# Kernel tuning notes

Measured on AMD Instinct MI355X. Metric: run time of the kernel, lower is better.

The kernel has to match this reference:

```python
import jax, jax.numpy as jnp
import numpy as np

B, T, N_EMBD, HEAD = 4, 4096, 1024, 64


def setup_inputs() -> dict:
    key = jax.random.key(0)
    kx, kk, kq, kv = jax.random.split(key, 4)
    x = jax.random.normal(kx, (B, T, N_EMBD), dtype=jnp.float32)
    s = 1.0 / np.sqrt(N_EMBD)  # init scale so activations stay O(1)
    Wk = jax.random.normal(kk, (N_EMBD, HEAD), dtype=jnp.float32) * s
    Wq = jax.random.normal(kq, (N_EMBD, HEAD), dtype=jnp.float32) * s
    Wv = jax.random.normal(kv, (N_EMBD, HEAD), dtype=jnp.float32) * s
    return {"x": x, "Wk": Wk, "Wq": Wq, "Wv": Wv}


def reference(x, Wk, Wq, Wv):
    Bd, Td, C = x.shape
    k = jnp.einsum('btc,ch->bth', x, Wk)
    q = jnp.einsum('btc,ch->bth', x, Wq)
    v = jnp.einsum('btc,ch->bth', x, Wv)
    # scores scaled by C**-0.5 where C = n_embd (as in the source, not head_size)
    w = jnp.einsum('bth,bsh->bts', q, k) * (C ** -0.5)
    causal = jnp.tril(jnp.ones((Td, Td), dtype=bool))  # [T, T]
    w = jnp.where(causal, w, -jnp.inf)
    w = jax.nn.softmax(w, axis=-1)
    out = jnp.einsum('bts,bsh->bth', w, v)  # [B, T, head_size]
    return out
```

## Files before the change

### kernel.cpp

```cpp
#include <hip/hip_runtime.h>
#include <cmath>

#define NB 4
#define NT 4096
#define NC 1024
#define NH 64
#define SCALE 0.03125f
#define MFIX 3.0f
#define LOG2E 1.4426950408889634f
#define QE 1048576

typedef __attribute__((ext_vector_type(8))) short v8s;
typedef __attribute__((ext_vector_type(4))) float f32x4;

static __device__ __forceinline__ ushort f2bf(float x) {
    union { float f; uint u; } c; c.f = x;
    return (ushort)((c.u + 0x7FFF + ((c.u >> 16) & 1)) >> 16);
}
static __device__ __forceinline__ uint pk2bf(float hi_f, float lo_f) {
    uint uh = __float_as_uint(hi_f) + 0x8000u;
    uint ul = __float_as_uint(lo_f) + 0x8000u;
    return __builtin_amdgcn_perm(uh, ul, 0x07060302u);
}

__global__ __launch_bounds__(256) void prep_kernel(
    const float* __restrict__ Wk, const float* __restrict__ Wq,
    const float* __restrict__ Wv, ushort* __restrict__ Wb)
{
    const int g    = blockIdx.x * 256 + threadIdx.x;
    const int lane = g & 63;
    const int kc   = (g >> 6) & 31;
    const int nt   = g >> 11;
    const int n    = nt * 16 + (lane & 15);
    const float* W = (n < 64) ? Wq : (n < 128) ? Wk : Wv;
    const int col  = n & 63;
    const int k0   = kc * 32 + ((lane >> 4) << 3);
    ushort t8[8];
    #pragma unroll
    for (int j = 0; j < 8; ++j)
        t8[j] = f2bf(W[(k0 + j) * 64 + col]);
    *(uint4*)(Wb + (size_t)g * 8) = *(const uint4*)t8;
}

#define PPAD 72

__global__ __launch_bounds__(256) void proj_kernel(
    const float* __restrict__ x, const ushort* __restrict__ Wb,
    ushort* __restrict__ qpack, ushort* __restrict__ kpack,
    ushort* __restrict__ vpack)
{
    __shared__ __align__(16) ushort As[2][32 * PPAD];
    __shared__ __align__(16) ushort Cs[32][200];

    const int tid  = threadIdx.x;
    const int w    = tid >> 6;
    const int lane = tid & 63;
    const int ln   = lane & 15;
    const int quad = lane >> 4;
    const long r0  = (long)blockIdx.x * 32;

    const int arow = tid >> 3, acol = (tid & 7) * 8;
    const float* xs = x + (r0 + arow) * NC + acol;

    const ushort* wb0 = Wb + (size_t)(w * 3 + 0) * 16384 + lane * 8;
    const ushort* wb1 = Wb + (size_t)(w * 3 + 1) * 16384 + lane * 8;
    const ushort* wb2 = Wb + (size_t)(w * 3 + 2) * 16384 + lane * 8;

    f32x4 acc[2][3];
    #pragma unroll
    for (int s = 0; s < 2; ++s)
        #pragma unroll
        for (int nt = 0; nt < 3; ++nt) acc[s][nt] = (f32x4){0.f,0.f,0.f,0.f};

    float4 f0 = *(const float4*)(xs);
    float4 f1 = *(const float4*)(xs + 4);
    float4 g0 = *(const float4*)(xs + 64);
    float4 g1 = *(const float4*)(xs + 68);
    v8s b[3][2];
    b[0][0] = *(const v8s*)(wb0);       b[0][1] = *(const v8s*)(wb0 + 512);
    b[1][0] = *(const v8s*)(wb1);       b[1][1] = *(const v8s*)(wb1 + 512);
    b[2][0] = *(const v8s*)(wb2);       b[2][1] = *(const v8s*)(wb2 + 512);
    {
        uint4 p = { pk2bf(f0.y, f0.x), pk2bf(f0.w, f0.z),
                    pk2bf(f1.y, f1.x), pk2bf(f1.w, f1.z) };
        *(uint4*)(&As[0][arow * PPAD + acol]) = p;
    }
    __syncthreads();

    int buf = 0;
    #pragma unroll
    for (int it = 0; it < 16; ++it) {
        float4 h0, h1;
        v8s nb[3][2];
        if (it < 14) {
            const int k2 = (it + 2) * 64;
            h0 = *(const float4*)(xs + k2);
            h1 = *(const float4*)(xs + k2 + 4);
        }
        if (it < 15) {
            const int off = (it + 1) * 1024;
            nb[0][0] = *(const v8s*)(wb0 + off); nb[0][1] = *(const v8s*)(wb0 + off + 512);
            nb[1][0] = *(const v8s*)(wb1 + off); nb[1][1] = *(const v8s*)(wb1 + off + 512);
            nb[2][0] = *(const v8s*)(wb2 + off); nb[2][1] = *(const v8s*)(wb2 + off + 512);
        }

        #pragma unroll
        for (int s = 0; s < 2; ++s) {
            const ushort* ap = &As[buf][(s * 16 + ln) * PPAD + quad * 8];
            v8s a0 = *(const v8s*)(ap);
            v8s a1 = *(const v8s*)(ap + 32);
            #pragma unroll
            for (int nt = 0; nt < 3; ++nt) {
                acc[s][nt] = __builtin_amdgcn_mfma_f32_16x16x32_bf16(a0, b[nt][0], acc[s][nt], 0, 0, 0);
                acc[s][nt] = __builtin_amdgcn_mfma_f32_16x16x32_bf16(a1, b[nt][1], acc[s][nt], 0, 0, 0);
            }
        }

        if (it < 15) {
            uint4 p = { pk2bf(g0.y, g0.x), pk2bf(g0.w, g0.z),
                        pk2bf(g1.y, g1.x), pk2bf(g1.w, g1.z) };
            *(uint4*)(&As[buf ^ 1][arow * PPAD + acol]) = p;
            #pragma unroll
            for (int nt = 0; nt < 3; ++nt) {
                b[nt][0] = nb[nt][0];
                b[nt][1] = nb[nt][1];
            }
        }
        if (it < 14) { g0 = h0; g1 = h1; }
        __syncthreads();
        buf ^= 1;
    }

    #pragma unroll
    for (int s = 0; s < 2; ++s)
        #pragma unroll
        for (int nt = 0; nt < 3; ++nt)
            #pragma unroll
            for (int r = 0; r < 4; ++r)
                Cs[s * 16 + quad * 4 + r][(w * 3 + nt) * 16 + ln] = f2bf(acc[s][nt][r]);
    __syncthreads();

    const int b_blk = (int)(r0 >> 12);
    const int t_loc = (int)(r0 & 4095);
    const int kt    = t_loc >> 6;
    const int kcb   = (t_loc >> 5) & 1;
    const int qt16a = t_loc >> 4;

    {
        const int f = tid >> 6, sx = f >> 1, kc = f & 1, lp = tid & 63;
        const int lnp = lp & 15, qdp = lp >> 4;
        const size_t fid = ((size_t)(b_blk * 256 + qt16a + sx) * 2 + kc);
        uint4 uq = *(const uint4*)(&Cs[sx * 16 + lnp][kc * 32 + qdp * 8]);
        *(uint4*)(qpack + fid * 512 + lp * 8) = uq;
        uint4 uk = *(const uint4*)(&Cs[sx * 16 + lnp][64 + kc * 32 + qdp * 8]);
        *(uint4*)(kpack + fid * 512 + lp * 8) = uk;
    }
    {
        const int td = tid >> 6, lp = tid & 63;
        const int lnv = lp & 15, qg = lp >> 4;
        ushort t8[8];
        #pragma unroll
        for (int j = 0; j < 8; ++j)
            t8[j] = Cs[qg * 8 + j][128 + td * 16 + lnv];
        const size_t fv = ((size_t)(b_blk * 64 + kt) * 2 + kcb) * 4 + td;
        *(uint4*)(vpack + fv * 512 + lp * 8) = *(const uint4*)t8;
    }
}

#define LPAD 40

__global__ __launch_bounds__(1024) void attn_kernel(
    const ushort* __restrict__ qpack, const ushort* __restrict__ kpack,
    const ushort* __restrict__ vpack, float* __restrict__ out)
{
    __shared__ __align__(16) ushort Ps[16][32 * LPAD];
    __shared__ __align__(16) float Obuf[8][32][68];
    __shared__ float Lbuf[8][32];

    const int id = blockIdx.x;
    const int j  = id >> 2;
    const int b  = id & 3;

    const int tid  = threadIdx.x;
    const int w    = tid >> 6;
    const int lane = tid & 63;
    const int ln   = lane & 15;
    const int quad = lane >> 4;

    const ushort* qpb = qpack + (size_t)b * 256 * 2 * 512 + lane * 8;
    const ushort* kpb = kpack + (size_t)b * 256 * 2 * 512 + lane * 8;
    const ushort* vpb = vpack + (size_t)b * 128 * 4 * 512 + lane * 8;

    ushort* Pw = &Ps[w][0];

    #pragma unroll
    for (int ph = 0; ph < 2; ++ph) {
        const int jp = ph ? (127 - j) : j;
        const int q0 = jp * 32;

        v8s qf[2][2];
        #pragma unroll
        for (int s = 0; s < 2; ++s) {
            qf[s][0] = *(const v8s*)(qpb + ((size_t)((jp * 2 + s) * 2 + 0)) * 512);
            qf[s][1] = *(const v8s*)(qpb + ((size_t)((jp * 2 + s) * 2 + 1)) * 512);
        }

        f32x4 o[2][4];
        #pragma unroll
        for (int s = 0; s < 2; ++s)
            #pragma unroll
            for (int td = 0; td < 4; ++td) o[s][td] = (f32x4){0.f,0.f,0.f,0.f};
        float l[2] = {0.f, 0.f};

        for (int kk = w; kk <= jp; kk += 16) {
            const ushort* kfb = kpb + (size_t)kk * 4 * 512;
            const ushort* vfb = vpb + (size_t)kk * 4 * 512;
            v8s K[4], V[4];
            #pragma unroll
            for (int i = 0; i < 4; ++i) K[i] = *(const v8s*)(kfb + i * 512);
            #pragma unroll
            for (int i = 0; i < 4; ++i) V[i] = *(const v8s*)(vfb + i * 512);
            const bool diag = (kk == jp);

            #pragma unroll
            for (int tk = 0; tk < 2; ++tk) {
                const int keybase = kk * 32 + tk * 16 + quad * 4;
                #pragma unroll
                for (int s = 0; s < 2; ++s) {
                    f32x4 acc = (f32x4){0.f,0.f,0.f,0.f};
                    acc = __builtin_amdgcn_mfma_f32_16x16x32_bf16(K[tk * 2 + 0], qf[s][0], acc, 0, 0, 0);
                    acc = __builtin_amdgcn_mfma_f32_16x16x32_bf16(K[tk * 2 + 1], qf[s][1], acc, 0, 0, 0);
                    const int qg = q0 + s * 16 + ln;
                    float p[4];
                    #pragma unroll
                    for (int r = 0; r < 4; ++r) {
                        float e = fmaf(acc[r], SCALE * LOG2E, -MFIX * LOG2E);
                        if (diag && (keybase + r > qg)) e = -1e30f;
                        p[r] = __builtin_amdgcn_exp2f(e);
                        l[s] += p[r];
                    }
                    uint2 pw = { pk2bf(p[1], p[0]), pk2bf(p[3], p[2]) };
                    *(uint2*)(&Pw[(s * 16 + ln) * LPAD + tk * 16 + quad * 4]) = pw;
                }
            }

            #pragma unroll
            for (int s = 0; s < 2; ++s) {
                v8s pf = *(const v8s*)(&Pw[(s * 16 + ln) * LPAD + quad * 8]);
                #pragma unroll
                for (int td = 0; td < 4; ++td)
                    o[s][td] = __builtin_amdgcn_mfma_f32_16x16x32_bf16(pf, V[td], o[s][td], 0, 0, 0);
            }
        }

        #pragma unroll
        for (int s = 0; s < 2; ++s) {
            l[s] += __shfl_xor(l[s], 16);
            l[s] += __shfl_xor(l[s], 32);
        }

        if (w >= 8) {
            #pragma unroll
            for (int s = 0; s < 2; ++s) {
                #pragma unroll
                for (int td = 0; td < 4; ++td)
                    #pragma unroll
                    for (int r = 0; r < 4; ++r)
                        Obuf[w - 8][s * 16 + quad * 4 + r][td * 16 + ln] = o[s][td][r];
                if (quad == 0) Lbuf[w - 8][s * 16 + ln] = l[s];
            }
        }
        __syncthreads();

        if (w < 8) {
            #pragma unroll
            for (int s = 0; s < 2; ++s) {
                l[s] += Lbuf[w][s * 16 + ln];
                #pragma unroll
                for (int td = 0; td < 4; ++td)
                    #pragma unroll
                    for (int r = 0; r < 4; ++r) {
                        float m = o[s][td][r] + Obuf[w][s * 16 + quad * 4 + r][td * 16 + ln];
                        Obuf[w][s * 16 + quad * 4 + r][td * 16 + ln] = m;
                    }
                if (quad == 0) Lbuf[w][s * 16 + ln] = l[s];
            }
        }
        __syncthreads();

        {
            const int qr = tid >> 5;
            const int h0 = (tid & 31) * 2;
            float s0 = 0.f, s1 = 0.f, Ls = 0.f;
            #pragma unroll
            for (int ww = 0; ww < 8; ++ww) {
                const float* Or = &Obuf[ww][qr][h0];
                s0 += Or[0]; s1 += Or[1];
                Ls += Lbuf[ww][qr];
            }
            const float inv = 1.0f / Ls;
            float2 r = { s0 * inv, s1 * inv };
            *(float2*)(out + ((size_t)b * NT + q0 + qr) * NH + h0) = r;
        }
        __syncthreads();
    }
}

extern "C" void kernel_launch(void* const* d_in, const int* in_sizes, int n_in,
                              void* d_out, int out_size, void* d_ws, size_t ws_size,
                              hipStream_t stream)
{
    const float* x  = (const float*)d_in[0];
    const float* Wk = (const float*)d_in[1];
    const float* Wq = (const float*)d_in[2];
    const float* Wv = (const float*)d_in[3];
    float* out = (float*)d_out;

    char* wsb = (char*)d_ws;
    ushort* qpack = (ushort*)wsb;
    ushort* kpack = qpack + QE;
    ushort* vpack = kpack + QE;
    ushort* Wb    = vpack + QE;

    prep_kernel<<<96, 256, 0, stream>>>(Wk, Wq, Wv, Wb);
    proj_kernel<<<NB * NT / 32, 256, 0, stream>>>(x, Wb, qpack, kpack, vpack);
    attn_kernel<<<64 * NB, 1024, 0, stream>>>(qpack, kpack, vpack, out);
}
```

Measured before the change: 127.8 us.

## Split attention into one query tile per 512-thread block with longest-first ordering

Instead of 256 blocks of 1024 threads that each handle a pair of query tiles (j and 127-j), the attention kernel now launches 512 blocks of 512 threads, each owning a single 32-row query tile. Blocks are ordered so the heaviest causal tiles are scheduled first, with a mirrored mapping for the second half. The cross-wave reduction now spans 8 waves and uses float4 output stores. The aim is finer-grained scheduling, higher occupancy via launch_bounds(512,4), and fewer barriers. The cost is more blocks and per-block setup, plus load balance that depends on the hardware scheduler instead of explicit pairing.

```diff
diff --git a/kernel.cpp b/kernel.cpp
--- a/kernel.cpp
+++ b/kernel.cpp
@@ -169,17 +169,19 @@
 
 #define LPAD 40
 
-__global__ __launch_bounds__(1024) void attn_kernel(
+__global__ __launch_bounds__(512, 4) void attn_kernel(
     const ushort* __restrict__ qpack, const ushort* __restrict__ kpack,
     const ushort* __restrict__ vpack, float* __restrict__ out)
 {
-    __shared__ __align__(16) ushort Ps[16][32 * LPAD];
-    __shared__ __align__(16) float Obuf[8][32][68];
-    __shared__ float Lbuf[8][32];
+    __shared__ __align__(16) ushort Ps[8][32 * LPAD];
+    __shared__ __align__(16) float Obuf[4][32][68];
+    __shared__ float Lbuf[4][32];
 
     const int id = blockIdx.x;
-    const int j  = id >> 2;
-    const int b  = id & 3;
+    const int r  = (id < 256) ? id : 767 - id;
+    const int jp = 127 - (r >> 2);
+    const int b  = r & 3;
+    const int q0 = jp * 32;
 
     const int tid  = threadIdx.x;
     const int w    = tid >> 6;
@@ -193,116 +195,110 @@
 
     ushort* Pw = &Ps[w][0];
 
-    #pragma unroll
-    for (int ph = 0; ph < 2; ++ph) {
-        const int jp = ph ? (127 - j) : j;
-        const int q0 = jp * 32;
-
-        v8s qf[2][2];
+    v8s qf[2][2];
+    #pragma unroll
+    for (int s = 0; s < 2; ++s) {
+        qf[s][0] = *(const v8s*)(qpb + ((size_t)((jp * 2 + s) * 2 + 0)) * 512);
+        qf[s][1] = *(const v8s*)(qpb + ((size_t)((jp * 2 + s) * 2 + 1)) * 512);
+    }
+
+    f32x4 o[2][4];
+    #pragma unroll
+    for (int s = 0; s < 2; ++s)
+        #pragma unroll
+        for (int td = 0; td < 4; ++td) o[s][td] = (f32x4){0.f,0.f,0.f,0.f};
+    float l[2] = {0.f, 0.f};
+
+    for (int kk = w; kk <= jp; kk += 8) {
+        const ushort* kfb = kpb + (size_t)kk * 4 * 512;
+        const ushort* vfb = vpb + (size_t)kk * 4 * 512;
+        v8s K[4], V[4];
+        #pragma unroll
+        for (int i = 0; i < 4; ++i) K[i] = *(const v8s*)(kfb + i * 512);
+        #pragma unroll
+        for (int i = 0; i < 4; ++i) V[i] = *(const v8s*)(vfb + i * 512);
+        const bool diag = (kk == jp);
+
+        #pragma unroll
+        for (int tk = 0; tk < 2; ++tk) {
+            const int keybase = kk * 32 + tk * 16 + quad * 4;
+            #pragma unroll
+            for (int s = 0; s < 2; ++s) {
+                f32x4 acc = (f32x4){0.f,0.f,0.f,0.f};
+                acc = __builtin_amdgcn_mfma_f32_16x16x32_bf16(K[tk * 2 + 0], qf[s][0], acc, 0, 0, 0);
+                acc = __builtin_amdgcn_mfma_f32_16x16x32_bf16(K[tk * 2 + 1], qf[s][1], acc, 0, 0, 0);
+                const int qg = q0 + s * 16 + ln;
+                float p[4];
+                #pragma unroll
+                for (int rr = 0; rr < 4; ++rr) {
+                    float e = fmaf(acc[rr], SCALE * LOG2E, -MFIX * LOG2E);
+                    if (diag && (keybase + rr > qg)) e = -1e30f;
+                    p[rr] = __builtin_amdgcn_exp2f(e);
+                    l[s] += p[rr];
+                }
+                uint2 pw = { pk2bf(p[1], p[0]), pk2bf(p[3], p[2]) };
+                *(uint2*)(&Pw[(s * 16 + ln) * LPAD + tk * 16 + quad * 4]) = pw;
+            }
+        }
+
         #pragma unroll
         for (int s = 0; s < 2; ++s) {
-            qf[s][0] = *(const v8s*)(qpb + ((size_t)((jp * 2 + s) * 2 + 0)) * 512);
-            qf[s][1] = *(const v8s*)(qpb + ((size_t)((jp * 2 + s) * 2 + 1)) * 512);
-        }
-
-        f32x4 o[2][4];
-        #pragma unroll
-        for (int s = 0; s < 2; ++s)
-            #pragma unroll
-            for (int td = 0; td < 4; ++td) o[s][td] = (f32x4){0.f,0.f,0.f,0.f};
-        float l[2] = {0.f, 0.f};
-
-        for (int kk = w; kk <= jp; kk += 16) {
-            const ushort* kfb = kpb + (size_t)kk * 4 * 512;
-            const ushort* vfb = vpb + (size_t)kk * 4 * 512;
-            v8s K[4], V[4];
-            #pragma unroll
-            for (int i = 0; i < 4; ++i) K[i] = *(const v8s*)(kfb + i * 512);
-            #pragma unroll
-            for (int i = 0; i < 4; ++i) V[i] = *(const v8s*)(vfb + i * 512);
-            const bool diag = (kk == jp);
-
-            #pragma unroll
-            for (int tk = 0; tk < 2; ++tk) {
-                const int keybase = kk * 32 + tk * 16 + quad * 4;
+            v8s pf = *(const v8s*)(&Pw[(s * 16 + ln) * LPAD + quad * 8]);
+            #pragma unroll
+            for (int td = 0; td < 4; ++td)
+                o[s][td] = __builtin_amdgcn_mfma_f32_16x16x32_bf16(pf, V[td], o[s][td], 0, 0, 0);
+        }
+    }
+
+    #pragma unroll
+    for (int s = 0; s < 2; ++s) {
+        l[s] += __shfl_xor(l[s], 16);
+        l[s] += __shfl_xor(l[s], 32);
+    }
+
+    if (w >= 4) {
+        #pragma unroll
+        for (int s = 0; s < 2; ++s) {
+            #pragma unroll
+            for (int td = 0; td < 4; ++td)
                 #pragma unroll
-                for (int s = 0; s < 2; ++s) {
-                    f32x4 acc = (f32x4){0.f,0.f,0.f,0.f};
-                    acc = __builtin_amdgcn_mfma_f32_16x16x32_bf16(K[tk * 2 + 0], qf[s][0], acc, 0, 0, 0);
-                    acc = __builtin_amdgcn_mfma_f32_16x16x32_bf16(K[tk * 2 + 1], qf[s][1], acc, 0, 0, 0);
-                    const int qg = q0 + s * 16 + ln;
-                    float p[4];
-                    #pragma unroll
-                    for (int r = 0; r < 4; ++r) {
-                        float e = fmaf(acc[r], SCALE * LOG2E, -MFIX * LOG2E);
-                        if (diag && (keybase + r > qg)) e = -1e30f;
-                        p[r] = __builtin_amdgcn_exp2f(e);
-                        l[s] += p[r];
-                    }
-                    uint2 pw = { pk2bf(p[1], p[0]), pk2bf(p[3], p[2]) };
-                    *(uint2*)(&Pw[(s * 16 + ln) * LPAD + tk * 16 + quad * 4]) = pw;
+                for (int rr = 0; rr < 4; ++rr)
+                    Obuf[w - 4][s * 16 + quad * 4 + rr][td * 16 + ln] = o[s][td][rr];
+            if (quad == 0) Lbuf[w - 4][s * 16 + ln] = l[s];
+        }
+    }
+    __syncthreads();
+
+    if (w < 4) {
+        #pragma unroll
+        for (int s = 0; s < 2; ++s) {
+            l[s] += Lbuf[w][s * 16 + ln];
+            #pragma unroll
+            for (int td = 0; td < 4; ++td)
+                #pragma unroll
+                for (int rr = 0; rr < 4; ++rr) {
+                    float m = o[s][td][rr] + Obuf[w][s * 16 + quad * 4 + rr][td * 16 + ln];
+                    Obuf[w][s * 16 + quad * 4 + rr][td * 16 + ln] = m;
                 }
-            }
-
-            #pragma unroll
-            for (int s = 0; s < 2; ++s) {
-                v8s pf = *(const v8s*)(&Pw[(s * 16 + ln) * LPAD + quad * 8]);
-                #pragma unroll
-                for (int td = 0; td < 4; ++td)
-                    o[s][td] = __builtin_amdgcn_mfma_f32_16x16x32_bf16(pf, V[td], o[s][td], 0, 0, 0);
-            }
-        }
-
-        #pragma unroll
-        for (int s = 0; s < 2; ++s) {
-            l[s] += __shfl_xor(l[s], 16);
-            l[s] += __shfl_xor(l[s], 32);
-        }
-
-        if (w >= 8) {
-            #pragma unroll
-            for (int s = 0; s < 2; ++s) {
-                #pragma unroll
-                for (int td = 0; td < 4; ++td)
-                    #pragma unroll
-                    for (int r = 0; r < 4; ++r)
-                        Obuf[w - 8][s * 16 + quad * 4 + r][td * 16 + ln] = o[s][td][r];
-                if (quad == 0) Lbuf[w - 8][s * 16 + ln] = l[s];
-            }
-        }
-        __syncthreads();
-
-        if (w < 8) {
-            #pragma unroll
-            for (int s = 0; s < 2; ++s) {
-                l[s] += Lbuf[w][s * 16 + ln];
-                #pragma unroll
-                for (int td = 0; td < 4; ++td)
-                    #pragma unroll
-                    for (int r = 0; r < 4; ++r) {
-                        float m = o[s][td][r] + Obuf[w][s * 16 + quad * 4 + r][td * 16 + ln];
-                        Obuf[w][s * 16 + quad * 4 + r][td * 16 + ln] = m;
-                    }
-                if (quad == 0) Lbuf[w][s * 16 + ln] = l[s];
-            }
-        }
-        __syncthreads();
-
-        {
-            const int qr = tid >> 5;
-            const int h0 = (tid & 31) * 2;
-            float s0 = 0.f, s1 = 0.f, Ls = 0.f;
-            #pragma unroll
-            for (int ww = 0; ww < 8; ++ww) {
-                const float* Or = &Obuf[ww][qr][h0];
-                s0 += Or[0]; s1 += Or[1];
-                Ls += Lbuf[ww][qr];
-            }
-            const float inv = 1.0f / Ls;
-            float2 r = { s0 * inv, s1 * inv };
-            *(float2*)(out + ((size_t)b * NT + q0 + qr) * NH + h0) = r;
-        }
-        __syncthreads();
+            if (quad == 0) Lbuf[w][s * 16 + ln] = l[s];
+        }
+    }
+    __syncthreads();
+
+    {
+        const int qr = tid >> 4;
+        const int h0 = (tid & 15) * 4;
+        float s0 = 0.f, s1 = 0.f, s2 = 0.f, s3 = 0.f, Ls = 0.f;
+        #pragma unroll
+        for (int ww = 0; ww < 4; ++ww) {
+            const float* Or = &Obuf[ww][qr][h0];
+            float4 u = *(const float4*)(Or);
+            s0 += u.x; s1 += u.y; s2 += u.z; s3 += u.w;
+            Ls += Lbuf[ww][qr];
+        }
+        const float inv = 1.0f / Ls;
+        float4 rv = { s0 * inv, s1 * inv, s2 * inv, s3 * inv };
+        *(float4*)(out + ((size_t)b * NT + q0 + qr) * NH + h0) = rv;
     }
 }
 
@@ -324,5 +320,5 @@
 
     prep_kernel<<<96, 256, 0, stream>>>(Wk, Wq, Wv, Wb);
     proj_kernel<<<NB * NT / 32, 256, 0, stream>>>(x, Wb, qpack, kpack, vpack);
-    attn_kernel<<<64 * NB, 1024, 0, stream>>>(qpack, kpack, vpack, out);
-}
+    attn_kernel<<<512, 512, 0, stream>>>(qpack, kpack, vpack, out);
+}
```

New measurement: 128.2 us. About the same (+0.3%).
